# Optimization experiments

Hardware: AMD Instinct MI355X
Metric: run time of the kernel (lower is better)

## Reference

```python
import jax, jax.numpy as jnp
import numpy as np

N = 50000      # nodes
E = 600000     # edges
D = 128        # hidden_dim (bottleneck=1)
G = 64         # graphs in batch
GN_EPS = 1e-5  # GraphNorm eps


def setup_inputs() -> dict:
    key = jax.random.key(0)
    ks = jax.random.split(key, 10)
    node_h = jax.random.normal(ks[0], (N, D), dtype=jnp.float32)
    edge_attr = jax.random.normal(ks[1], (E, D), dtype=jnp.float32)
    batch = jnp.sort(jax.random.randint(ks[2], (N,), 0, G)).astype(jnp.int64)
    edge_index = jax.random.randint(ks[3], (2, E), 0, N).astype(jnp.int64)
    # params: lin1, conv.lin (edge linear), conv.eps, GraphNorm(weight,bias,mean_scale)
    w1 = jax.random.normal(ks[4], (D, D), dtype=jnp.float32) * 0.02
    b1 = jnp.zeros((D,), dtype=jnp.float32)
    we = jax.random.normal(ks[5], (D, D), dtype=jnp.float32) * 0.02
    be = jnp.zeros((D,), dtype=jnp.float32)
    eps = jnp.zeros((), dtype=jnp.float32)  # train_eps, init 0
    gn_weight = jnp.ones((D,), dtype=jnp.float32)
    gn_bias = jnp.zeros((D,), dtype=jnp.float32)
    gn_mean_scale = jnp.ones((D,), dtype=jnp.float32)
    return {"node_h": node_h, "edge_attr": edge_attr, "batch": batch,
            "edge_index": edge_index, "w1": w1, "b1": b1, "we": we, "be": be,
            "eps": eps, "gn_weight": gn_weight, "gn_bias": gn_bias,
            "gn_mean_scale": gn_mean_scale}


def graph_norm(x, batch, weight, bias, mean_scale):
    ones = jnp.ones((x.shape[0],), dtype=x.dtype)
    cnt = jnp.maximum(jax.ops.segment_sum(ones, batch, num_segments=G), 1.0)[:, None]
    mean = jax.ops.segment_sum(x, batch, num_segments=G) / cnt
    out = x - mean[batch] * mean_scale
    var = jax.ops.segment_sum(out * out, batch, num_segments=G) / cnt
    std = jnp.sqrt(var + GN_EPS)
    return weight * out / std[batch] + bias


def reference(node_h, edge_attr, batch, edge_index, w1, b1, we, be, eps,
              gn_weight, gn_bias, gn_mean_scale):
    h = node_h @ w1.T + b1                                  # lin1: [N, D]
    src, dst = edge_index[0], edge_index[1]
    # GINEConvMod message: SiLU(x_j + lin(edge_attr)); gather -> add -> act
    msg = jax.nn.silu(h[src] + (edge_attr @ we.T + be))     # [E, D]
    agg = jax.ops.segment_sum(msg, dst, num_segments=N)     # scatter-add
    conv = (1.0 + eps) * h + agg                            # nn = Identity
    # dropout(p=0) and lin2=Identity are no-ops
    out = jax.nn.silu(conv)
    return graph_norm(out + node_h, batch, gn_weight, gn_bias, gn_mean_scale)
```

## Files before the change

kernel.cpp:

```cpp
#include <hip/hip_runtime.h>
#include <hip/hip_bf16.h>

#define NN 50000
#define NE 600000
#define DIM 128
#define NG 64
#define NCHUNK 98

using bf16x8 = __attribute__((ext_vector_type(8))) __bf16;
using bf16x4 = __attribute__((ext_vector_type(4))) __bf16;
using f32x4  = __attribute__((ext_vector_type(4))) float;

__device__ __forceinline__ bf16x8 cvt8(const float* __restrict__ p) {
    f32x4 a = *(const f32x4*)p;
    f32x4 b = *(const f32x4*)(p + 4);
    bf16x8 r;
    #pragma unroll
    for (int i = 0; i < 4; ++i) { r[i] = (__bf16)a[i]; r[i + 4] = (__bf16)b[i]; }
    return r;
}

template<int NT>
__device__ __forceinline__ void stage_weights_swz(const float* __restrict__ W, __bf16* sW) {
    for (int i = threadIdx.x; i < 128 * 16; i += NT) {
        int row = i >> 4, seg = i & 15;
        *(bf16x8*)(&sW[row * 128 + ((seg ^ (row & 15)) << 3)]) = cvt8(W + row * 128 + seg * 8);
    }
    __syncthreads();
}

__device__ __forceinline__ bf16x8 ldsA(const __bf16* sW, int t, int col, int quad, int k0) {
    int chunk = ((k0 >> 3) + quad) ^ col;
    return *(const bf16x8*)(&sW[(t * 16 + col) * 128 + (chunk << 3)]);
}

__global__ __launch_bounds__(512) void gemm_bias(
    const float* __restrict__ X, const float* __restrict__ W,
    const float* __restrict__ bias, float* __restrict__ Y, int M)
{
    __shared__ __bf16 sW[128 * 128];
    stage_weights_swz<512>(W, sW);

    int wave = threadIdx.x >> 6, lane = threadIdx.x & 63;
    int col = lane & 15, quad = lane >> 4;
    int tile = (blockIdx.x * 8 + wave) * 16;
    if (tile >= M) return;

    f32x4 acc[8] = {};
    const float* xp = X + (size_t)(tile + col) * DIM + quad * 8;
    #pragma unroll
    for (int k0 = 0; k0 < 128; k0 += 32) {
        bf16x8 b = cvt8(xp + k0);
        #pragma unroll
        for (int t = 0; t < 8; ++t) {
            bf16x8 a = ldsA(sW, t, col, quad, k0);
            acc[t] = __builtin_amdgcn_mfma_f32_16x16x32_bf16(a, b, acc[t], 0, 0, 0);
        }
    }
    float* yp = Y + (size_t)(tile + col) * DIM + quad * 4;
    #pragma unroll
    for (int t = 0; t < 8; ++t) {
        f32x4 bv = *(const f32x4*)(bias + t * 16 + quad * 4);
        f32x4 o;
        #pragma unroll
        for (int r = 0; r < 4; ++r) o[r] = acc[t][r] + bv[r];
        *(f32x4*)(yp + t * 16) = o;
    }
}

__global__ __launch_bounds__(256) void k_hist(const int* __restrict__ dst, int* __restrict__ deg) {
    int e = blockIdx.x * 256 + threadIdx.x;
    if (e < NE) atomicAdd(&deg[dst[e]], 1);
}

__global__ __launch_bounds__(256) void k_scan_a(const int* __restrict__ deg, int* __restrict__ chunkSum) {
    __shared__ int s[256];
    int c = blockIdx.x, t = threadIdx.x;
    int b = c * 512 + t;
    int v = (b < NN) ? deg[b] : 0;
    if (b + 256 < NN) v += deg[b + 256];
    s[t] = v; __syncthreads();
    for (int off = 128; off > 0; off >>= 1) {
        if (t < off) s[t] += s[t + off];
        __syncthreads();
    }
    if (t == 0) chunkSum[c] = s[0];
}

__global__ __launch_bounds__(128) void k_scan_b(const int* __restrict__ chunkSum,
                                                int* __restrict__ chunkOff, int* __restrict__ rowptr) {
    __shared__ int s[128];
    int t = threadIdx.x;
    int v = (t < NCHUNK) ? chunkSum[t] : 0;
    s[t] = v; __syncthreads();
    for (int off = 1; off < 128; off <<= 1) {
        int x = (t >= off) ? s[t - off] : 0;
        __syncthreads();
        s[t] += x;
        __syncthreads();
    }
    chunkOff[t] = s[t] - v;
    if (t == 0) rowptr[NN] = NE;
}

__global__ __launch_bounds__(512) void k_scan_c(const int* __restrict__ deg,
                                                const int* __restrict__ chunkOff,
                                                int* __restrict__ rowptr, int* __restrict__ pos) {
    __shared__ int s[512];
    int c = blockIdx.x, t = threadIdx.x;
    int i = c * 512 + t;
    int v = (i < NN) ? deg[i] : 0;
    s[t] = v; __syncthreads();
    for (int off = 1; off < 512; off <<= 1) {
        int x = (t >= off) ? s[t - off] : 0;
        __syncthreads();
        s[t] += x;
        __syncthreads();
    }
    if (i < NN) { rowptr[i] = chunkOff[c] + s[t] - v; pos[i] = 0; }
}

__global__ __launch_bounds__(256) void k_slot(const int* __restrict__ dst,
                                              const int* __restrict__ rowptr,
                                              int* __restrict__ pos, int* __restrict__ slot) {
    int e = blockIdx.x * 256 + threadIdx.x;
    if (e >= NE) return;
    int d = dst[e];
    int p = atomicAdd(&pos[d], 1);
    slot[e] = rowptr[d] + p;
}

__global__ __launch_bounds__(512) void edge_msg_sorted(
    const float* __restrict__ EA, const float* __restrict__ W,
    const float* __restrict__ bias,
    const int* __restrict__ src, const int* __restrict__ slot,
    const float* __restrict__ H, __hip_bfloat16* __restrict__ MSG)
{
    __shared__ __bf16 sW[128 * 128];

    int wave = threadIdx.x >> 6, lane = threadIdx.x & 63;
    int col = lane & 15, quad = lane >> 4;
    int tile = (blockIdx.x * 8 + wave) * 16;
    bool active = (tile < NE);
    int e  = active ? (tile + col) : 0;

    int s  = src[e];
    int sl = slot[e];

    stage_weights_swz<512>(W, sW);
    if (!active) return;

    f32x4 acc[8] = {};
    const float* xp = EA + (size_t)e * DIM + quad * 8;
    #pragma unroll
    for (int k0 = 0; k0 < 128; k0 += 32) {
        bf16x8 b = cvt8(xp + k0);
        #pragma unroll
        for (int t = 0; t < 8; ++t) {
            bf16x8 a = ldsA(sW, t, col, quad, k0);
            acc[t] = __builtin_amdgcn_mfma_f32_16x16x32_bf16(a, b, acc[t], 0, 0, 0);
        }
    }

    const float* hp = H + (size_t)s * DIM + quad * 4;
    f32x4 hv[8];
    #pragma unroll
    for (int t = 0; t < 8; ++t) hv[t] = *(const f32x4*)(hp + t * 16);

    __hip_bfloat16* mp = MSG + (size_t)sl * DIM + quad * 4;
    #pragma unroll
    for (int t = 0; t < 8; ++t) {
        f32x4 bv = *(const f32x4*)(bias + t * 16 + quad * 4);
        bf16x4 o;
        #pragma unroll
        for (int r = 0; r < 4; ++r) {
            float v = acc[t][r] + bv[r] + hv[t][r];
            v = v / (1.f + __expf(-v));
            o[r] = (__bf16)v;
        }
        *(bf16x4*)(mp + t * 16) = o;
    }
}

__global__ __launch_bounds__(128) void k_gather(
    const __hip_bfloat16* __restrict__ MSG, const int* __restrict__ rowptr,
    float* __restrict__ H, const float* __restrict__ node_h,
    const float* __restrict__ epsp)
{
    int n = blockIdx.x, d = threadIdx.x;
    int s = rowptr[n], epos = rowptr[n + 1];
    const __hip_bfloat16* mp = MSG + (size_t)s * DIM + d;
    float a0 = 0.f, a1 = 0.f, a2 = 0.f, a3 = 0.f;
    int e = s;
    for (; e + 4 <= epos; e += 4, mp += 4 * DIM) {
        a0 += __bfloat162float(mp[0]);
        a1 += __bfloat162float(mp[DIM]);
        a2 += __bfloat162float(mp[2 * DIM]);
        a3 += __bfloat162float(mp[3 * DIM]);
    }
    for (; e < epos; ++e, mp += DIM) a0 += __bfloat162float(mp[0]);
    float acc = (a0 + a1) + (a2 + a3);
    size_t idx = (size_t)n * DIM + d;
    float v = (1.f + epsp[0]) * H[idx] + acc;
    v = v / (1.f + __expf(-v));
    H[idx] = v + node_h[idx];
}

__global__ __launch_bounds__(128) void stats_pass(
    const float* __restrict__ X, const int* __restrict__ batch,
    float* __restrict__ SUMS, float* __restrict__ SQS,
    float* __restrict__ CNT, int npb)
{
    int d = threadIdx.x;
    int n0 = blockIdx.x * npb;
    int nend = min(n0 + npb, NN);
    if (n0 >= NN) return;
    int cur_g = batch[n0];
    float run = 0.f, run2 = 0.f; int runlen = 0;
    for (int n = n0; n < nend; ++n) {
        int g = batch[n];
        if (g != cur_g) {
            atomicAdd(&SUMS[cur_g * DIM + d], run);
            atomicAdd(&SQS[cur_g * DIM + d], run2);
            if (d == 0) atomicAdd(&CNT[cur_g], (float)runlen);
            run = 0.f; run2 = 0.f; runlen = 0; cur_g = g;
        }
        float x = X[(size_t)n * DIM + d];
        run += x; run2 += x * x; runlen++;
    }
    atomicAdd(&SUMS[cur_g * DIM + d], run);
    atomicAdd(&SQS[cur_g * DIM + d], run2);
    if (d == 0) atomicAdd(&CNT[cur_g], (float)runlen);
}

__global__ __launch_bounds__(128) void finalize(
    const float* __restrict__ X, const int* __restrict__ batch,
    const float* __restrict__ msc,
    const float* __restrict__ SUMS, const float* __restrict__ SQS,
    const float* __restrict__ CNT,
    const float* __restrict__ gw, const float* __restrict__ gb,
    float* __restrict__ OUT, int npb)
{
    int d = threadIdx.x;
    int n0 = blockIdx.x * npb;
    int nend = min(n0 + npb, NN);
    if (n0 >= NN) return;
    float ms = msc[d], wd = gw[d], bd = gb[d];
    int cur_g = -1;
    float mean = 0.f, rstd = 0.f;
    for (int n = n0; n < nend; ++n) {
        int g = batch[n];
        if (g != cur_g) {
            cur_g = g;
            float c = fmaxf(CNT[g], 1.f);
            mean = SUMS[g * DIM + d] / c;
            float ex2 = SQS[g * DIM + d] / c;
            float var = ex2 - mean * mean * ms * (2.f - ms);
            rstd = rsqrtf(fmaxf(var, 0.f) + 1e-5f);
        }
        size_t idx = (size_t)n * DIM + d;
        float v = X[idx] - mean * ms;
        OUT[idx] = wd * v * rstd + bd;
    }
}

__global__ __launch_bounds__(512) void edge_msg_atomic(
    const float* __restrict__ EA, const float* __restrict__ W,
    const float* __restrict__ bias,
    const int* __restrict__ src, const int* __restrict__ dst,
    const float* __restrict__ H, float* __restrict__ AGG)
{
    __shared__ __bf16 sW[128 * 128];
    int wave = threadIdx.x >> 6, lane = threadIdx.x & 63;
    int col = lane & 15, quad = lane >> 4;
    int tile = (blockIdx.x * 8 + wave) * 16;
    bool active = (tile < NE);
    int e = active ? (tile + col) : 0;
    int s = src[e], dd = dst[e];

    stage_weights_swz<512>(W, sW);
    if (!active) return;

    f32x4 acc[8] = {};
    const float* xp = EA + (size_t)e * DIM + quad * 8;
    #pragma unroll
    for (int k0 = 0; k0 < 128; k0 += 32) {
        bf16x8 b = cvt8(xp + k0);
        #pragma unroll
        for (int t = 0; t < 8; ++t) {
            bf16x8 a = ldsA(sW, t, col, quad, k0);
            acc[t] = __builtin_amdgcn_mfma_f32_16x16x32_bf16(a, b, acc[t], 0, 0, 0);
        }
    }
    const float* hp = H + (size_t)s * DIM + quad * 4;
    f32x4 hv[8];
    #pragma unroll
    for (int t = 0; t < 8; ++t) hv[t] = *(const f32x4*)(hp + t * 16);

    float* ap = AGG + (size_t)dd * DIM + quad * 4;
    #pragma unroll
    for (int t = 0; t < 8; ++t) {
        f32x4 bv = *(const f32x4*)(bias + t * 16 + quad * 4);
        #pragma unroll
        for (int r = 0; r < 4; ++r) {
            float v = acc[t][r] + bv[r] + hv[t][r];
            v = v / (1.f + __expf(-v));
            atomicAdd(&ap[t * 16 + r], v);
        }
    }
}

__global__ __launch_bounds__(128) void fuse_x_atomic(
    float* __restrict__ H, const float* __restrict__ AGG,
    const float* __restrict__ node_h, const float* __restrict__ epsp, int npb)
{
    int d = threadIdx.x;
    int n0 = blockIdx.x * npb;
    int nend = min(n0 + npb, NN);
    if (n0 >= NN) return;
    float epsv = 1.f + epsp[0];
    for (int n = n0; n < nend; ++n) {
        size_t idx = (size_t)n * DIM + d;
        float v = epsv * H[idx] + AGG[idx];
        v = v / (1.f + __expf(-v));
        H[idx] = v + node_h[idx];
    }
}

extern "C" void kernel_launch(void* const* d_in, const int* in_sizes, int n_in,
                              void* d_out, int out_size, void* d_ws, size_t ws_size,
                              hipStream_t stream) {
    const float* node_h    = (const float*)d_in[0];
    const float* edge_attr = (const float*)d_in[1];
    const int*   batch     = (const int*)d_in[2];
    const int*   eidx      = (const int*)d_in[3];
    const float* w1        = (const float*)d_in[4];
    const float* b1        = (const float*)d_in[5];
    const float* we        = (const float*)d_in[6];
    const float* be        = (const float*)d_in[7];
    const float* eps       = (const float*)d_in[8];
    const float* gnw       = (const float*)d_in[9];
    const float* gnb       = (const float*)d_in[10];
    const float* gnms      = (const float*)d_in[11];
    const int* src = eidx, * dst = eidx + NE;

    char* base = (char*)d_ws;
    float* H = (float*)base;

    size_t oMSG   = 25600000;
    size_t oROW   = oMSG + 153600000;
    size_t oDEG   = oROW + 200064;
    size_t oSUMS  = oDEG + 200000;
    size_t oSQS   = oSUMS + 32768;
    size_t oCNT   = oSQS + 32768;
    size_t oSLOT  = oCNT + 256;
    size_t oCSA   = oSLOT + 2400000;
    size_t oCSB   = oCSA + 512;
    size_t needed = oCSB + 512;

    bool fast = ws_size >= needed;

    if (fast) {
        __hip_bfloat16* MSG = (__hip_bfloat16*)(base + oMSG);
        int* rowptr = (int*)(base + oROW);
        int* deg    = (int*)(base + oDEG);
        float* SUMS = (float*)(base + oSUMS);
        float* SQS  = (float*)(base + oSQS);
        float* CNT  = (float*)(base + oCNT);
        int* slot   = (int*)(base + oSLOT);
        int* csum   = (int*)(base + oCSA);
        int* coff   = (int*)(base + oCSB);

        hipMemsetAsync(deg, 0, 200000 + 32768 + 32768 + 256, stream);

        gemm_bias<<<391, 512, 0, stream>>>(node_h, w1, b1, H, NN);
        k_hist  <<<(NE + 255) / 256, 256, 0, stream>>>(dst, deg);
        k_scan_a<<<NCHUNK, 256, 0, stream>>>(deg, csum);
        k_scan_b<<<1, 128, 0, stream>>>(csum, coff, rowptr);
        k_scan_c<<<NCHUNK, 512, 0, stream>>>(deg, coff, rowptr, deg );
        k_slot  <<<(NE + 255) / 256, 256, 0, stream>>>(dst, rowptr, deg, slot);
        edge_msg_sorted<<<4688, 512, 0, stream>>>(edge_attr, we, be, src, slot, H, MSG);
        k_gather<<<NN, 128, 0, stream>>>(MSG, rowptr, H, node_h, eps);
        stats_pass<<<3125, 128, 0, stream>>>(H, batch, SUMS, SQS, CNT, 16);
        finalize  <<<3125, 128, 0, stream>>>(H, batch, gnms, SUMS, SQS, CNT, gnw, gnb,
                                             (float*)d_out, 16);
    } else {
        float* AGG  = H + 6400000;
        float* SUMS = H + 12800000;
        float* SQS  = SUMS + NG * DIM;
        float* CNT  = SQS + NG * DIM;
        hipMemsetAsync(AGG, 0, (size_t)(6400000 + NG * DIM * 2 + NG) * sizeof(float), stream);
        gemm_bias<<<391, 512, 0, stream>>>(node_h, w1, b1, H, NN);
        edge_msg_atomic<<<4688, 512, 0, stream>>>(edge_attr, we, be, src, dst, H, AGG);
        fuse_x_atomic<<<3125, 128, 0, stream>>>(H, AGG, node_h, eps, 16);
        stats_pass<<<3125, 128, 0, stream>>>(H, batch, SUMS, SQS, CNT, 16);
        finalize  <<<3125, 128, 0, stream>>>(H, batch, gnms, SUMS, SQS, CNT, gnw, gnb,
                                             (float*)d_out, 16);
    }
}
```

Before: 682.0 us.

## Gather bf16 H copy in edge messages, persist edge kernel, fuse gather into stats

The node linear kernel now also writes a bf16 copy of H in a lane-friendly permuted layout, and the edge message kernel gathers source rows from it, halving gather bytes. The edge kernel becomes a grid-stride persistent kernel so the weight tile is staged into LDS once per block rather than once per 128 edges. The CSR aggregation, residual and SiLU are fused into the GraphNorm statistics pass, removing a full read of H and a launch. The cost is lower parallelism in the fused gather (each block walks 16 nodes serially), plus bf16 rounding of h in the message.

```diff
diff --git a/kernel.cpp b/kernel.cpp
--- a/kernel.cpp
+++ b/kernel.cpp
@@ -6,6 +6,8 @@
 #define DIM 128
 #define NG 64
 #define NCHUNK 98
+#define NTILE_E 37500
+#define EDGE_BLOCKS 1024
 
 using bf16x8 = __attribute__((ext_vector_type(8))) __bf16;
 using bf16x4 = __attribute__((ext_vector_type(4))) __bf16;
@@ -36,7 +38,8 @@
 
 __global__ __launch_bounds__(512) void gemm_bias(
     const float* __restrict__ X, const float* __restrict__ W,
-    const float* __restrict__ bias, float* __restrict__ Y, int M)
+    const float* __restrict__ bias, float* __restrict__ Y,
+    __hip_bfloat16* __restrict__ Yb, int M)
 {
     __shared__ __bf16 sW[128 * 128];
     stage_weights_swz<512>(W, sW);
@@ -65,6 +68,21 @@
         #pragma unroll
         for (int r = 0; r < 4; ++r) o[r] = acc[t][r] + bv[r];
         *(f32x4*)(yp + t * 16) = o;
+        #pragma unroll
+        for (int r = 0; r < 4; ++r) acc[t][r] = o[r];
+    }
+    if (Yb) {
+        __hip_bfloat16* ybp = Yb + (size_t)(tile + col) * DIM + quad * 32;
+        #pragma unroll
+        for (int tp = 0; tp < 4; ++tp) {
+            bf16x8 o8;
+            #pragma unroll
+            for (int r = 0; r < 4; ++r) {
+                o8[r]     = (__bf16)acc[2 * tp][r];
+                o8[4 + r] = (__bf16)acc[2 * tp + 1][r];
+            }
+            *(bf16x8*)(ybp + tp * 8) = o8;
+        }
     }
 }
 
@@ -134,80 +152,58 @@
     const float* __restrict__ EA, const float* __restrict__ W,
     const float* __restrict__ bias,
     const int* __restrict__ src, const int* __restrict__ slot,
-    const float* __restrict__ H, __hip_bfloat16* __restrict__ MSG)
+    const __hip_bfloat16* __restrict__ Hb, __hip_bfloat16* __restrict__ MSG)
 {
     __shared__ __bf16 sW[128 * 128];
+    stage_weights_swz<512>(W, sW);
 
     int wave = threadIdx.x >> 6, lane = threadIdx.x & 63;
     int col = lane & 15, quad = lane >> 4;
-    int tile = (blockIdx.x * 8 + wave) * 16;
-    bool active = (tile < NE);
-    int e  = active ? (tile + col) : 0;
-
-    int s  = src[e];
-    int sl = slot[e];
-
-    stage_weights_swz<512>(W, sW);
-    if (!active) return;
-
-    f32x4 acc[8] = {};
-    const float* xp = EA + (size_t)e * DIM + quad * 8;
-    #pragma unroll
-    for (int k0 = 0; k0 < 128; k0 += 32) {
-        bf16x8 b = cvt8(xp + k0);
+    int wstride = gridDim.x * 8;
+
+    for (int ti = blockIdx.x * 8 + wave; ti < NTILE_E; ti += wstride) {
+        int e  = ti * 16 + col;
+        int s  = src[e];
+        int sl = slot[e];
+
+        f32x4 acc[8] = {};
+        const float* xp = EA + (size_t)e * DIM + quad * 8;
+        #pragma unroll
+        for (int k0 = 0; k0 < 128; k0 += 32) {
+            bf16x8 b = cvt8(xp + k0);
+            #pragma unroll
+            for (int t = 0; t < 8; ++t) {
+                bf16x8 a = ldsA(sW, t, col, quad, k0);
+                acc[t] = __builtin_amdgcn_mfma_f32_16x16x32_bf16(a, b, acc[t], 0, 0, 0);
+            }
+        }
+
+        const __hip_bfloat16* hp = Hb + (size_t)s * DIM + quad * 32;
+        bf16x8 hv4[4];
+        #pragma unroll
+        for (int tp = 0; tp < 4; ++tp) hv4[tp] = *(const bf16x8*)(hp + tp * 8);
+
+        __hip_bfloat16* mp = MSG + (size_t)sl * DIM + quad * 4;
         #pragma unroll
         for (int t = 0; t < 8; ++t) {
-            bf16x8 a = ldsA(sW, t, col, quad, k0);
-            acc[t] = __builtin_amdgcn_mfma_f32_16x16x32_bf16(a, b, acc[t], 0, 0, 0);
-        }
-    }
-
-    const float* hp = H + (size_t)s * DIM + quad * 4;
-    f32x4 hv[8];
-    #pragma unroll
-    for (int t = 0; t < 8; ++t) hv[t] = *(const f32x4*)(hp + t * 16);
-
-    __hip_bfloat16* mp = MSG + (size_t)sl * DIM + quad * 4;
-    #pragma unroll
-    for (int t = 0; t < 8; ++t) {
-        f32x4 bv = *(const f32x4*)(bias + t * 16 + quad * 4);
-        bf16x4 o;
-        #pragma unroll
-        for (int r = 0; r < 4; ++r) {
-            float v = acc[t][r] + bv[r] + hv[t][r];
-            v = v / (1.f + __expf(-v));
-            o[r] = (__bf16)v;
-        }
-        *(bf16x4*)(mp + t * 16) = o;
-    }
-}
-
-__global__ __launch_bounds__(128) void k_gather(
+            f32x4 bv = *(const f32x4*)(bias + t * 16 + quad * 4);
+            bf16x4 o;
+            #pragma unroll
+            for (int r = 0; r < 4; ++r) {
+                float hf = __bfloat162float((__hip_bfloat16)hv4[t >> 1][(t & 1) * 4 + r]);
+                float v = acc[t][r] + bv[r] + hf;
+                v = v / (1.f + __expf(-v));
+                o[r] = (__bf16)v;
+            }
+            *(bf16x4*)(mp + t * 16) = o;
+        }
+    }
+}
+
+__global__ __launch_bounds__(128) void k_gather_stats(
     const __hip_bfloat16* __restrict__ MSG, const int* __restrict__ rowptr,
     float* __restrict__ H, const float* __restrict__ node_h,
-    const float* __restrict__ epsp)
-{
-    int n = blockIdx.x, d = threadIdx.x;
-    int s = rowptr[n], epos = rowptr[n + 1];
-    const __hip_bfloat16* mp = MSG + (size_t)s * DIM + d;
-    float a0 = 0.f, a1 = 0.f, a2 = 0.f, a3 = 0.f;
-    int e = s;
-    for (; e + 4 <= epos; e += 4, mp += 4 * DIM) {
-        a0 += __bfloat162float(mp[0]);
-        a1 += __bfloat162float(mp[DIM]);
-        a2 += __bfloat162float(mp[2 * DIM]);
-        a3 += __bfloat162float(mp[3 * DIM]);
-    }
-    for (; e < epos; ++e, mp += DIM) a0 += __bfloat162float(mp[0]);
-    float acc = (a0 + a1) + (a2 + a3);
-    size_t idx = (size_t)n * DIM + d;
-    float v = (1.f + epsp[0]) * H[idx] + acc;
-    v = v / (1.f + __expf(-v));
-    H[idx] = v + node_h[idx];
-}
-
-__global__ __launch_bounds__(128) void stats_pass(
-    const float* __restrict__ X, const int* __restrict__ batch,
+    const float* __restrict__ epsp, const int* __restrict__ batch,
     float* __restrict__ SUMS, float* __restrict__ SQS,
     float* __restrict__ CNT, int npb)
 {
@@ -215,6 +211,7 @@
     int n0 = blockIdx.x * npb;
     int nend = min(n0 + npb, NN);
     if (n0 >= NN) return;
+    float epsv = 1.f + epsp[0];
     int cur_g = batch[n0];
     float run = 0.f, run2 = 0.f; int runlen = 0;
     for (int n = n0; n < nend; ++n) {
@@ -225,8 +222,24 @@
             if (d == 0) atomicAdd(&CNT[cur_g], (float)runlen);
             run = 0.f; run2 = 0.f; runlen = 0; cur_g = g;
         }
-        float x = X[(size_t)n * DIM + d];
-        run += x; run2 += x * x; runlen++;
+        int s = rowptr[n], epos = rowptr[n + 1];
+        const __hip_bfloat16* mp = MSG + (size_t)s * DIM + d;
+        float a0 = 0.f, a1 = 0.f, a2 = 0.f, a3 = 0.f;
+        int e = s;
+        for (; e + 4 <= epos; e += 4, mp += 4 * DIM) {
+            a0 += __bfloat162float(mp[0]);
+            a1 += __bfloat162float(mp[DIM]);
+            a2 += __bfloat162float(mp[2 * DIM]);
+            a3 += __bfloat162float(mp[3 * DIM]);
+        }
+        for (; e < epos; ++e, mp += DIM) a0 += __bfloat162float(mp[0]);
+        float agg = (a0 + a1) + (a2 + a3);
+        size_t idx = (size_t)n * DIM + d;
+        float v = epsv * H[idx] + agg;
+        v = v / (1.f + __expf(-v));
+        v += node_h[idx];
+        H[idx] = v;
+        run += v; run2 += v * v; runlen++;
     }
     atomicAdd(&SUMS[cur_g * DIM + d], run);
     atomicAdd(&SQS[cur_g * DIM + d], run2);
@@ -264,6 +277,33 @@
     }
 }
 
+__global__ __launch_bounds__(128) void stats_pass(
+    const float* __restrict__ X, const int* __restrict__ batch,
+    float* __restrict__ SUMS, float* __restrict__ SQS,
+    float* __restrict__ CNT, int npb)
+{
+    int d = threadIdx.x;
+    int n0 = blockIdx.x * npb;
+    int nend = min(n0 + npb, NN);
+    if (n0 >= NN) return;
+    int cur_g = batch[n0];
+    float run = 0.f, run2 = 0.f; int runlen = 0;
+    for (int n = n0; n < nend; ++n) {
+        int g = batch[n];
+        if (g != cur_g) {
+            atomicAdd(&SUMS[cur_g * DIM + d], run);
+            atomicAdd(&SQS[cur_g * DIM + d], run2);
+            if (d == 0) atomicAdd(&CNT[cur_g], (float)runlen);
+            run = 0.f; run2 = 0.f; runlen = 0; cur_g = g;
+        }
+        float x = X[(size_t)n * DIM + d];
+        run += x; run2 += x * x; runlen++;
+    }
+    atomicAdd(&SUMS[cur_g * DIM + d], run);
+    atomicAdd(&SQS[cur_g * DIM + d], run2);
+    if (d == 0) atomicAdd(&CNT[cur_g], (float)runlen);
+}
+
 __global__ __launch_bounds__(512) void edge_msg_atomic(
     const float* __restrict__ EA, const float* __restrict__ W,
     const float* __restrict__ bias,
@@ -356,7 +396,8 @@
     size_t oSLOT  = oCNT + 256;
     size_t oCSA   = oSLOT + 2400000;
     size_t oCSB   = oCSA + 512;
-    size_t needed = oCSB + 512;
+    size_t oHB    = oCSB + 512;
+    size_t needed = oHB + 12800000;
 
     bool fast = ws_size >= needed;
 
@@ -370,27 +411,28 @@
         int* slot   = (int*)(base + oSLOT);
         int* csum   = (int*)(base + oCSA);
         int* coff   = (int*)(base + oCSB);
+        __hip_bfloat16* Hb = (__hip_bfloat16*)(base + oHB);
 
         hipMemsetAsync(deg, 0, 200000 + 32768 + 32768 + 256, stream);
 
-        gemm_bias<<<391, 512, 0, stream>>>(node_h, w1, b1, H, NN);
+        gemm_bias<<<391, 512, 0, stream>>>(node_h, w1, b1, H, Hb, NN);
         k_hist  <<<(NE + 255) / 256, 256, 0, stream>>>(dst, deg);
         k_scan_a<<<NCHUNK, 256, 0, stream>>>(deg, csum);
         k_scan_b<<<1, 128, 0, stream>>>(csum, coff, rowptr);
         k_scan_c<<<NCHUNK, 512, 0, stream>>>(deg, coff, rowptr, deg );
         k_slot  <<<(NE + 255) / 256, 256, 0, stream>>>(dst, rowptr, deg, slot);
-        edge_msg_sorted<<<4688, 512, 0, stream>>>(edge_attr, we, be, src, slot, H, MSG);
-        k_gather<<<NN, 128, 0, stream>>>(MSG, rowptr, H, node_h, eps);
-        stats_pass<<<3125, 128, 0, stream>>>(H, batch, SUMS, SQS, CNT, 16);
-        finalize  <<<3125, 128, 0, stream>>>(H, batch, gnms, SUMS, SQS, CNT, gnw, gnb,
-                                             (float*)d_out, 16);
+        edge_msg_sorted<<<EDGE_BLOCKS, 512, 0, stream>>>(edge_attr, we, be, src, slot, Hb, MSG);
+        k_gather_stats<<<3125, 128, 0, stream>>>(MSG, rowptr, H, node_h, eps, batch,
+                                                 SUMS, SQS, CNT, 16);
+        finalize<<<3125, 128, 0, stream>>>(H, batch, gnms, SUMS, SQS, CNT, gnw, gnb,
+                                           (float*)d_out, 16);
     } else {
         float* AGG  = H + 6400000;
         float* SUMS = H + 12800000;
         float* SQS  = SUMS + NG * DIM;
         float* CNT  = SQS + NG * DIM;
         hipMemsetAsync(AGG, 0, (size_t)(6400000 + NG * DIM * 2 + NG) * sizeof(float), stream);
-        gemm_bias<<<391, 512, 0, stream>>>(node_h, w1, b1, H, NN);
+        gemm_bias<<<391, 512, 0, stream>>>(node_h, w1, b1, H, nullptr, NN);
         edge_msg_atomic<<<4688, 512, 0, stream>>>(edge_attr, we, be, src, dst, H, AGG);
         fuse_x_atomic<<<3125, 128, 0, stream>>>(H, AGG, node_h, eps, 16);
         stats_pass<<<3125, 128, 0, stream>>>(H, batch, SUMS, SQS, CNT, 16);
```

Result: faster. 660.4 us (-3.2%).
